# Performance work log

Measured on AMD Instinct MI355X. Metric: run time of the kernel, lower is better.

The kernel has to match this reference:

```python
import jax, jax.numpy as jnp
import numpy as np

B, L, D = 8, 8192, 1024
M = L // 4  # target_ratio=4 -> exactly L/4 boundaries per batch row (enforced in setup_inputs)


@jax.custom_vjp
def ste(x):
    # Forward: ones_like(x). Backward: pass gradient straight through.
    return jnp.ones_like(x)

def _ste_fwd(x):
    return jnp.ones_like(x), None

def _ste_bwd(_, g):
    return (g,)

ste.defvjp(_ste_fwd, _ste_bwd)


def _ema_combine(c1, c2):
    # Linear recurrence h = a*h_prev + b as an associative op (matches the
    # Hillis-Steele doubling scan in the torch source exactly).
    a1, b1 = c1
    a2, b2 = c2
    return (a1 * a2, a2[..., None] * b1 + b2)


def setup_inputs() -> dict:
    key = jax.random.key(0)
    k1, k2, k3, k4, k5 = jax.random.split(key, 5)
    x = jax.random.normal(k1, (B, L, D), jnp.float32)
    residual = jax.random.normal(k2, (B, L, D), jnp.float32)
    prob = jax.random.uniform(k3, (B, L), jnp.float32)
    # exactly M=L//4 True positions per row (random locations) -> static M
    r = jax.random.uniform(k4, (B, L))
    sel = jnp.argsort(r, axis=1)[:, :M]
    token_mask = jnp.zeros((B, L), bool).at[jnp.arange(B)[:, None], sel].set(True)
    state = jax.random.normal(k5, (B, D), jnp.float32)
    return {"x": x, "residual": residual, "prob": prob,
            "token_mask": token_mask, "state": state}


def reference(x, residual, prob, token_mask, state):
    # ---- Tokenizer: compact selected positions to the front (stable order) ----
    counts = token_mask.sum(axis=1)                       # (B,)
    order = jnp.argsort(~token_mask, axis=1)[:, :M]       # stable: True positions first, in order
    chunked = jnp.take_along_axis(x, order[:, :, None], axis=1)      # (B, M, D)
    chunk_probs = jnp.take_along_axis(prob, order, axis=1)           # (B, M)
    valid = jnp.arange(M)[None, :] < counts[:, None]                  # (B, M)
    chunk_probs = chunk_probs * valid                     # padded slots -> 0 (new_zeros semantics)

    # ---- EMA scan over compacted chunks ----
    decay = jnp.clip(1.0 - chunk_probs, 0.0, 1.0)         # (B, M)
    b = (1.0 - decay)[..., None] * chunked                # (B, M, D)
    b = b.at[:, 0].add(decay[:, 0, None] * state)         # fold initial state into b[0]
    _, ema = jax.lax.associative_scan(_ema_combine, (decay, b), axis=1)
    ema = ema * valid[..., None]

    # ---- DeTokenizer: scatter-expand back to (B, L, D) ----
    chunk_idx = jnp.cumsum(token_mask.astype(jnp.int32), axis=1) - 1  # (B, L)
    valid_pos = chunk_idx >= 0
    ci = jnp.clip(chunk_idx, 0, M - 1)
    long_states = jnp.take_along_axis(ema, ci[:, :, None], axis=1)    # (B, L, D)
    long_states = long_states * valid_pos[..., None]

    coef = ste(jnp.maximum(1.0 - prob, prob))             # forward: ones; bwd: STE
    long_states = long_states * coef[..., None]

    output = residual + long_states                       # (B, L, D)

    # new_state = last valid EMA value per batch (or carried-over state if empty)
    last = jnp.clip(counts - 1, 0, M - 1)
    new_state = jnp.take_along_axis(ema, last[:, None, None], axis=1)[:, 0]
    new_state = jnp.where((counts > 0)[:, None], new_state, state)
    return output, new_state
```

## Files before the change

### kernel.cpp

```cpp
#include <hip/hip_runtime.h>
#include <stdint.h>
#include <stddef.h>

#define B_ 8
#define L_ 8192
#define D_ 1024
#define M_ 2048
#define S_ 128
#define G_ 16
#define D4_ (D_/4)

typedef float f4 __attribute__((ext_vector_type(4)));

#define OFF_POS    ((size_t)0)
#define OFF_DEC    (OFF_POS  + (size_t)B_*M_*4)
#define OFF_A      (OFF_DEC  + (size_t)B_*M_*4)
#define OFF_EZ     (OFF_A    + (size_t)B_*S_*4)
#define OFF_HINIT  (OFF_EZ   + (size_t)B_*S_*D_*4)
#define WS_TOTAL   (OFF_HINIT + (size_t)B_*S_*D_*4)

__global__ __launch_bounds__(1024)
void compact_kernel(const void* __restrict__ mask_raw,
                    const float* __restrict__ prob,
                    int* __restrict__ pos,
                    float* __restrict__ dec) {
    const int b = blockIdx.x;
    const int t = threadIdx.x;

    __shared__ int u8flag;
    if (t == 0) u8flag = 0;
    __syncthreads();
    {
        const uint32_t* mu = (const uint32_t*)mask_raw;
        uint32_t w0 = mu[t * 2], w1 = mu[t * 2 + 1];
        if (w0 > 1u || w1 > 1u) atomicOr(&u8flag, 1);
    }
    __syncthreads();
    const bool u8 = (u8flag != 0);

    int mv[8];
    const int base_l = t * 8;
    if (u8) {
        const uint8_t* mrow = (const uint8_t*)mask_raw + (size_t)b * L_;
        #pragma unroll
        for (int j = 0; j < 8; j++) mv[j] = mrow[base_l + j] ? 1 : 0;
    } else {
        const int* mrow = (const int*)mask_raw + (size_t)b * L_;
        #pragma unroll
        for (int j = 0; j < 8; j++) mv[j] = mrow[base_l + j] ? 1 : 0;
    }
    int tsum = 0;
    #pragma unroll
    for (int j = 0; j < 8; j++) tsum += mv[j];

    const int lane = t & 63, wid = t >> 6;
    int v = tsum;
    #pragma unroll
    for (int off = 1; off < 64; off <<= 1) {
        int n = __shfl_up(v, off, 64);
        if (lane >= off) v += n;
    }
    __shared__ int wsum[16];
    __shared__ int woff[16];
    if (lane == 63) wsum[wid] = v;
    __syncthreads();
    if (t < 16) {
        int acc = 0;
        for (int w = 0; w < t; w++) acc += wsum[w];
        woff[t] = acc;
    }
    __syncthreads();
    int run = (v - tsum) + woff[wid];

    const float* prow = prob + (size_t)b * L_;
    #pragma unroll
    for (int j = 0; j < 8; j++) {
        const int l = base_l + j;
        if (mv[j]) {
            float d = 1.0f - prow[l];
            d = fminf(fmaxf(d, 0.0f), 1.0f);
            pos[(size_t)b * M_ + run] = l;
            dec[(size_t)b * M_ + run] = d;
            run += 1;
        }
    }
}

__global__ __launch_bounds__(256)
void segend_kernel(const f4* __restrict__ x4,
                   const int* __restrict__ pos,
                   const float* __restrict__ dec,
                   f4* __restrict__ ez4,
                   float* __restrict__ Aseg) {
    const int blk = blockIdx.x;
    const int b = blk / S_, s = blk % S_;
    const int t = threadIdx.x;
    __shared__ int   pl[G_];
    __shared__ float dl[G_];
    if (t < G_) {
        pl[t] = pos[(size_t)b * M_ + (size_t)s * G_ + t];
        dl[t] = dec[(size_t)b * M_ + (size_t)s * G_ + t];
    }
    __syncthreads();
    f4 h = (f4)(0.0f);
    #pragma unroll
    for (int m = 0; m < G_; m++) {
        const float d = dl[m];
        const float w = 1.0f - d;
        const f4 xv = x4[((size_t)b * L_ + pl[m]) * D4_ + t];
        h = d * h + w * xv;
    }
    ez4[((size_t)b * S_ + s) * D4_ + t] = h;
    if (t == 0) {
        float p = 1.0f;
        #pragma unroll
        for (int m = 0; m < G_; m++) p *= dl[m];
        Aseg[b * S_ + s] = p;
    }
}

__global__ __launch_bounds__(64)
void combine_kernel(const float* __restrict__ ez,
                    const float* __restrict__ Aseg,
                    const float* __restrict__ state,
                    float* __restrict__ hinit,
                    float* __restrict__ newstate) {
    const int b = blockIdx.x;
    const int ch = blockIdx.y * 64 + threadIdx.x;
    __shared__ float Al[S_];
    Al[threadIdx.x] = Aseg[b * S_ + threadIdx.x];
    Al[threadIdx.x + 64] = Aseg[b * S_ + threadIdx.x + 64];
    __syncthreads();

    float c = state[(size_t)b * D_ + ch];
    for (int s0 = 0; s0 < S_; s0 += 8) {
        float e[8];
        #pragma unroll
        for (int j = 0; j < 8; j++)
            e[j] = ez[((size_t)b * S_ + s0 + j) * D_ + ch];
        #pragma unroll
        for (int j = 0; j < 8; j++) {
            hinit[((size_t)b * S_ + s0 + j) * D_ + ch] = c;
            c = fmaf(Al[s0 + j], c, e[j]);
        }
    }
    newstate[(size_t)b * D_ + ch] = c;
}

__global__ __launch_bounds__(256)
void fused_kernel(const f4* __restrict__ x4,
                  const f4* __restrict__ res4,
                  const int* __restrict__ pos,
                  const float* __restrict__ dec,
                  const f4* __restrict__ hinit4,
                  f4* __restrict__ out4) {
    const int blk = blockIdx.x;
    const int b = blk / S_, s = blk % S_;
    const int t = threadIdx.x;
    __shared__ int   pl[G_ + 1];
    __shared__ float dl[G_];
    if (t < G_) {
        pl[t] = pos[(size_t)b * M_ + (size_t)s * G_ + t];
        dl[t] = dec[(size_t)b * M_ + (size_t)s * G_ + t];
    }
    if (t == 0) {
        pl[G_] = (s == S_ - 1) ? L_ : pos[(size_t)b * M_ + (size_t)(s + 1) * G_];
    }
    __syncthreads();

    const f4* xrow   = x4   + (size_t)b * L_ * D4_;
    const f4* resrow = res4 + (size_t)b * L_ * D4_;
    f4*       outrow = out4 + (size_t)b * L_ * D4_;

    if (s == 0) {
        const int p0 = pl[0];
        int l = 0;
        for (; l + 4 <= p0; l += 4) {
            f4 r0 = __builtin_nontemporal_load(resrow + (size_t)(l + 0) * D4_ + t);
            f4 r1 = __builtin_nontemporal_load(resrow + (size_t)(l + 1) * D4_ + t);
            f4 r2 = __builtin_nontemporal_load(resrow + (size_t)(l + 2) * D4_ + t);
            f4 r3 = __builtin_nontemporal_load(resrow + (size_t)(l + 3) * D4_ + t);
            __builtin_nontemporal_store(r0, outrow + (size_t)(l + 0) * D4_ + t);
            __builtin_nontemporal_store(r1, outrow + (size_t)(l + 1) * D4_ + t);
            __builtin_nontemporal_store(r2, outrow + (size_t)(l + 2) * D4_ + t);
            __builtin_nontemporal_store(r3, outrow + (size_t)(l + 3) * D4_ + t);
        }
        for (; l < p0; l++) {
            f4 r = __builtin_nontemporal_load(resrow + (size_t)l * D4_ + t);
            __builtin_nontemporal_store(r, outrow + (size_t)l * D4_ + t);
        }
    }

    f4 h  = hinit4[((size_t)b * S_ + s) * D4_ + t];
    f4 xv = xrow[(size_t)pl[0] * D4_ + t];
    for (int m = 0; m < G_; m++) {
        f4 xn = xv;
        if (m < G_ - 1) xn = xrow[(size_t)pl[m + 1] * D4_ + t];
        const float d = dl[m];
        const float w = 1.0f - d;
        h = d * h + w * xv;
        const int lend = pl[m + 1];
        int l = pl[m];
        for (; l + 4 <= lend; l += 4) {
            f4 r0 = __builtin_nontemporal_load(resrow + (size_t)(l + 0) * D4_ + t);
            f4 r1 = __builtin_nontemporal_load(resrow + (size_t)(l + 1) * D4_ + t);
            f4 r2 = __builtin_nontemporal_load(resrow + (size_t)(l + 2) * D4_ + t);
            f4 r3 = __builtin_nontemporal_load(resrow + (size_t)(l + 3) * D4_ + t);
            r0 += h; r1 += h; r2 += h; r3 += h;
            __builtin_nontemporal_store(r0, outrow + (size_t)(l + 0) * D4_ + t);
            __builtin_nontemporal_store(r1, outrow + (size_t)(l + 1) * D4_ + t);
            __builtin_nontemporal_store(r2, outrow + (size_t)(l + 2) * D4_ + t);
            __builtin_nontemporal_store(r3, outrow + (size_t)(l + 3) * D4_ + t);
        }
        for (; l < lend; l++) {
            f4 r = __builtin_nontemporal_load(resrow + (size_t)l * D4_ + t);
            r += h;
            __builtin_nontemporal_store(r, outrow + (size_t)l * D4_ + t);
        }
        xv = xn;
    }
}

extern "C" void kernel_launch(void* const* d_in, const int* in_sizes, int n_in,
                              void* d_out, int out_size, void* d_ws, size_t ws_size,
                              hipStream_t stream) {
    const float* x        = (const float*)d_in[0];
    const float* residual = (const float*)d_in[1];
    const float* prob     = (const float*)d_in[2];
    const void*  mask     = d_in[3];
    const float* state    = (const float*)d_in[4];

    float* out       = (float*)d_out;
    float* new_state = out + (size_t)B_ * L_ * D_;

    if (ws_size < WS_TOTAL) return;

    char* ws = (char*)d_ws;
    int*   pos   = (int*)  (ws + OFF_POS);
    float* dec   = (float*)(ws + OFF_DEC);
    float* Aseg  = (float*)(ws + OFF_A);
    float* ez    = (float*)(ws + OFF_EZ);
    float* hinit = (float*)(ws + OFF_HINIT);

    compact_kernel<<<B_, 1024, 0, stream>>>(mask, prob, pos, dec);

    segend_kernel<<<B_ * S_, 256, 0, stream>>>(
        (const f4*)x, pos, dec, (f4*)ez, Aseg);

    combine_kernel<<<dim3(B_, 16), 64, 0, stream>>>(
        ez, Aseg, state, hinit, new_state);

    fused_kernel<<<B_ * S_, 256, 0, stream>>>(
        (const f4*)x, (const f4*)residual, pos, dec,
        (const f4*)hinit, (f4*)out);
}
```

Measured before the change: 147.4 us.

## Fuse four-stage pipeline into one cooperative kernel with grid syncs

Result: slower. 480.7 us (+226.2%).

```diff
diff --git a/kernel.cpp b/kernel.cpp
--- a/kernel.cpp
+++ b/kernel.cpp
@@ -1,6 +1,9 @@
 #include <hip/hip_runtime.h>
+#include <hip/hip_cooperative_groups.h>
 #include <stdint.h>
 #include <stddef.h>
+
+namespace cg = cooperative_groups;
 
 #define B_ 8
 #define L_ 8192
@@ -9,6 +12,7 @@
 #define S_ 128
 #define G_ 16
 #define D4_ (D_/4)
+#define NBLK_ (B_*S_)
 
 typedef float f4 __attribute__((ext_vector_type(4)));
 
@@ -18,6 +22,192 @@
 #define OFF_EZ     (OFF_A    + (size_t)B_*S_*4)
 #define OFF_HINIT  (OFF_EZ   + (size_t)B_*S_*D_*4)
 #define WS_TOTAL   (OFF_HINIT + (size_t)B_*S_*D_*4)
+
+__global__ __launch_bounds__(256, 4)
+void mega_kernel(const f4* __restrict__ x4,
+                 const f4* __restrict__ res4,
+                 const float* __restrict__ prob,
+                 const void* __restrict__ mask_raw,
+                 const float* __restrict__ state,
+                 int* __restrict__ pos,
+                 float* __restrict__ dec,
+                 float* __restrict__ Aseg,
+                 float* __restrict__ ez,
+                 float* __restrict__ hinit,
+                 f4* __restrict__ out4,
+                 float* __restrict__ newstate) {
+    cg::grid_group grid = cg::this_grid();
+    const int blk = blockIdx.x;
+    const int t = threadIdx.x;
+
+    __shared__ int   u8flag;
+    __shared__ int   wsum[4];
+    __shared__ int   woff[4];
+    __shared__ int   pl[G_ + 1];
+    __shared__ float dl[G_];
+    __shared__ float Al[S_];
+
+    if (blk < B_) {
+        const int b = blk;
+        if (t == 0) u8flag = 0;
+        __syncthreads();
+        {
+            const uint32_t* mu = (const uint32_t*)mask_raw;
+            uint32_t orv = 0;
+            #pragma unroll
+            for (int j = 0; j < 8; j++) orv |= mu[t * 8 + j];
+            if (orv > 1u) atomicOr(&u8flag, 1);
+        }
+        __syncthreads();
+        const bool u8 = (u8flag != 0);
+
+        const int base_l = t * 32;
+        int cnt = 0;
+        if (u8) {
+            const uint8_t* mrow = (const uint8_t*)mask_raw + (size_t)b * L_;
+            #pragma unroll
+            for (int j = 0; j < 32; j++) cnt += mrow[base_l + j] ? 1 : 0;
+        } else {
+            const int* mrow = (const int*)mask_raw + (size_t)b * L_;
+            #pragma unroll
+            for (int j = 0; j < 32; j++) cnt += mrow[base_l + j] ? 1 : 0;
+        }
+        const int lane = t & 63, wid = t >> 6;
+        int v = cnt;
+        #pragma unroll
+        for (int off = 1; off < 64; off <<= 1) {
+            int n = __shfl_up(v, off, 64);
+            if (lane >= off) v += n;
+        }
+        if (lane == 63) wsum[wid] = v;
+        __syncthreads();
+        if (t < 4) {
+            int acc = 0;
+            for (int w = 0; w < t; w++) acc += wsum[w];
+            woff[t] = acc;
+        }
+        __syncthreads();
+        int run = (v - cnt) + woff[wid];
+
+        const float* prow = prob + (size_t)b * L_;
+        if (u8) {
+            const uint8_t* mrow = (const uint8_t*)mask_raw + (size_t)b * L_;
+            for (int j = 0; j < 32; j++) {
+                const int l = base_l + j;
+                if (mrow[l]) {
+                    float d = fminf(fmaxf(1.0f - prow[l], 0.0f), 1.0f);
+                    pos[(size_t)b * M_ + run] = l;
+                    dec[(size_t)b * M_ + run] = d;
+                    run++;
+                }
+            }
+        } else {
+            const int* mrow = (const int*)mask_raw + (size_t)b * L_;
+            for (int j = 0; j < 32; j++) {
+                const int l = base_l + j;
+                if (mrow[l]) {
+                    float d = fminf(fmaxf(1.0f - prow[l], 0.0f), 1.0f);
+                    pos[(size_t)b * M_ + run] = l;
+                    dec[(size_t)b * M_ + run] = d;
+                    run++;
+                }
+            }
+        }
+        __threadfence();
+    }
+    grid.sync();
+
+    const int b = blk >> 7;
+    const int s = blk & (S_ - 1);
+    if (t < G_) {
+        pl[t] = pos[(size_t)b * M_ + s * G_ + t];
+        dl[t] = dec[(size_t)b * M_ + s * G_ + t];
+    }
+    if (t == 0) {
+        pl[G_] = (s == S_ - 1) ? L_ : pos[(size_t)b * M_ + (s + 1) * G_];
+    }
+    __syncthreads();
+
+    const f4* xrow = x4 + (size_t)b * L_ * D4_;
+    f4 xr[G_];
+    f4 h = (f4)(0.0f);
+    #pragma unroll
+    for (int m = 0; m < G_; m++) {
+        xr[m] = xrow[(size_t)pl[m] * D4_ + t];
+        const float d = dl[m];
+        h = d * h + (1.0f - d) * xr[m];
+    }
+    ((f4*)ez)[(size_t)blk * D4_ + t] = h;
+    if (t == 0) {
+        float p = 1.0f;
+        #pragma unroll
+        for (int m = 0; m < G_; m++) p *= dl[m];
+        Aseg[blk] = p;
+    }
+    __threadfence();
+    grid.sync();
+
+    if (blk < 32) {
+        const int b2 = blk >> 2;
+        const int ch = ((blk & 3) << 8) + t;
+        if (t < S_) Al[t] = Aseg[b2 * S_ + t];
+        __syncthreads();
+        float c = state[(size_t)b2 * D_ + ch];
+        for (int s0 = 0; s0 < S_; s0 += 8) {
+            float e[8];
+            #pragma unroll
+            for (int j = 0; j < 8; j++)
+                e[j] = ez[((size_t)b2 * S_ + s0 + j) * D_ + ch];
+            #pragma unroll
+            for (int j = 0; j < 8; j++) {
+                hinit[((size_t)b2 * S_ + s0 + j) * D_ + ch] = c;
+                c = fmaf(Al[s0 + j], c, e[j]);
+            }
+        }
+        newstate[(size_t)b2 * D_ + ch] = c;
+        __threadfence();
+    }
+    grid.sync();
+
+    const f4* resrow = res4 + (size_t)b * L_ * D4_;
+    f4*       outrow = out4 + (size_t)b * L_ * D4_;
+
+    if (s == 0) {
+        const int p0 = pl[0];
+        int l = 0;
+        for (; l + 2 <= p0; l += 2) {
+            f4 r0 = __builtin_nontemporal_load(resrow + (size_t)(l + 0) * D4_ + t);
+            f4 r1 = __builtin_nontemporal_load(resrow + (size_t)(l + 1) * D4_ + t);
+            __builtin_nontemporal_store(r0, outrow + (size_t)(l + 0) * D4_ + t);
+            __builtin_nontemporal_store(r1, outrow + (size_t)(l + 1) * D4_ + t);
+        }
+        if (l < p0) {
+            f4 r = __builtin_nontemporal_load(resrow + (size_t)l * D4_ + t);
+            __builtin_nontemporal_store(r, outrow + (size_t)l * D4_ + t);
+        }
+    }
+
+    f4 h3 = ((const f4*)hinit)[(size_t)blk * D4_ + t];
+    #pragma unroll
+    for (int m = 0; m < G_; m++) {
+        const float d = dl[m];
+        h3 = d * h3 + (1.0f - d) * xr[m];
+        const int lend = pl[m + 1];
+        int l = pl[m];
+        for (; l + 2 <= lend; l += 2) {
+            f4 r0 = __builtin_nontemporal_load(resrow + (size_t)(l + 0) * D4_ + t);
+            f4 r1 = __builtin_nontemporal_load(resrow + (size_t)(l + 1) * D4_ + t);
+            r0 += h3; r1 += h3;
+            __builtin_nontemporal_store(r0, outrow + (size_t)(l + 0) * D4_ + t);
+            __builtin_nontemporal_store(r1, outrow + (size_t)(l + 1) * D4_ + t);
+        }
+        if (l < lend) {
+            f4 r = __builtin_nontemporal_load(resrow + (size_t)l * D4_ + t);
+            r += h3;
+            __builtin_nontemporal_store(r, outrow + (size_t)l * D4_ + t);
+        }
+    }
+}
 
 __global__ __launch_bounds__(1024)
 void compact_kernel(const void* __restrict__ mask_raw,
@@ -26,7 +216,6 @@
                     float* __restrict__ dec) {
     const int b = blockIdx.x;
     const int t = threadIdx.x;
-
     __shared__ int u8flag;
     if (t == 0) u8flag = 0;
     __syncthreads();
@@ -37,7 +226,6 @@
     }
     __syncthreads();
     const bool u8 = (u8flag != 0);
-
     int mv[8];
     const int base_l = t * 8;
     if (u8) {
@@ -52,7 +240,6 @@
     int tsum = 0;
     #pragma unroll
     for (int j = 0; j < 8; j++) tsum += mv[j];
-
     const int lane = t & 63, wid = t >> 6;
     int v = tsum;
     #pragma unroll
@@ -71,14 +258,12 @@
     }
     __syncthreads();
     int run = (v - tsum) + woff[wid];
-
     const float* prow = prob + (size_t)b * L_;
     #pragma unroll
     for (int j = 0; j < 8; j++) {
         const int l = base_l + j;
         if (mv[j]) {
-            float d = 1.0f - prow[l];
-            d = fminf(fmaxf(d, 0.0f), 1.0f);
+            float d = fminf(fmaxf(1.0f - prow[l], 0.0f), 1.0f);
             pos[(size_t)b * M_ + run] = l;
             dec[(size_t)b * M_ + run] = d;
             run += 1;
@@ -106,9 +291,8 @@
     #pragma unroll
     for (int m = 0; m < G_; m++) {
         const float d = dl[m];
-        const float w = 1.0f - d;
         const f4 xv = x4[((size_t)b * L_ + pl[m]) * D4_ + t];
-        h = d * h + w * xv;
+        h = d * h + (1.0f - d) * xv;
     }
     ez4[((size_t)b * S_ + s) * D4_ + t] = h;
     if (t == 0) {
@@ -131,7 +315,6 @@
     Al[threadIdx.x] = Aseg[b * S_ + threadIdx.x];
     Al[threadIdx.x + 64] = Aseg[b * S_ + threadIdx.x + 64];
     __syncthreads();
-
     float c = state[(size_t)b * D_ + ch];
     for (int s0 = 0; s0 < S_; s0 += 8) {
         float e[8];
@@ -167,57 +350,28 @@
         pl[G_] = (s == S_ - 1) ? L_ : pos[(size_t)b * M_ + (size_t)(s + 1) * G_];
     }
     __syncthreads();
-
     const f4* xrow   = x4   + (size_t)b * L_ * D4_;
     const f4* resrow = res4 + (size_t)b * L_ * D4_;
     f4*       outrow = out4 + (size_t)b * L_ * D4_;
-
     if (s == 0) {
         const int p0 = pl[0];
-        int l = 0;
-        for (; l + 4 <= p0; l += 4) {
-            f4 r0 = __builtin_nontemporal_load(resrow + (size_t)(l + 0) * D4_ + t);
-            f4 r1 = __builtin_nontemporal_load(resrow + (size_t)(l + 1) * D4_ + t);
-            f4 r2 = __builtin_nontemporal_load(resrow + (size_t)(l + 2) * D4_ + t);
-            f4 r3 = __builtin_nontemporal_load(resrow + (size_t)(l + 3) * D4_ + t);
-            __builtin_nontemporal_store(r0, outrow + (size_t)(l + 0) * D4_ + t);
-            __builtin_nontemporal_store(r1, outrow + (size_t)(l + 1) * D4_ + t);
-            __builtin_nontemporal_store(r2, outrow + (size_t)(l + 2) * D4_ + t);
-            __builtin_nontemporal_store(r3, outrow + (size_t)(l + 3) * D4_ + t);
-        }
-        for (; l < p0; l++) {
+        for (int l = 0; l < p0; l++) {
             f4 r = __builtin_nontemporal_load(resrow + (size_t)l * D4_ + t);
             __builtin_nontemporal_store(r, outrow + (size_t)l * D4_ + t);
         }
     }
-
-    f4 h  = hinit4[((size_t)b * S_ + s) * D4_ + t];
-    f4 xv = xrow[(size_t)pl[0] * D4_ + t];
+    f4 h = hinit4[((size_t)b * S_ + s) * D4_ + t];
+    #pragma unroll
     for (int m = 0; m < G_; m++) {
-        f4 xn = xv;
-        if (m < G_ - 1) xn = xrow[(size_t)pl[m + 1] * D4_ + t];
         const float d = dl[m];
-        const float w = 1.0f - d;
-        h = d * h + w * xv;
+        const f4 xv = xrow[(size_t)pl[m] * D4_ + t];
+        h = d * h + (1.0f - d) * xv;
         const int lend = pl[m + 1];
-        int l = pl[m];
-        for (; l + 4 <= lend; l += 4) {
-            f4 r0 = __builtin_nontemporal_load(resrow + (size_t)(l + 0) * D4_ + t);
-            f4 r1 = __builtin_nontemporal_load(resrow + (size_t)(l + 1) * D4_ + t);
-            f4 r2 = __builtin_nontemporal_load(resrow + (size_t)(l + 2) * D4_ + t);
-            f4 r3 = __builtin_nontemporal_load(resrow + (size_t)(l + 3) * D4_ + t);
-            r0 += h; r1 += h; r2 += h; r3 += h;
-            __builtin_nontemporal_store(r0, outrow + (size_t)(l + 0) * D4_ + t);
-            __builtin_nontemporal_store(r1, outrow + (size_t)(l + 1) * D4_ + t);
-            __builtin_nontemporal_store(r2, outrow + (size_t)(l + 2) * D4_ + t);
-            __builtin_nontemporal_store(r3, outrow + (size_t)(l + 3) * D4_ + t);
-        }
-        for (; l < lend; l++) {
+        for (int l = pl[m]; l < lend; l++) {
             f4 r = __builtin_nontemporal_load(resrow + (size_t)l * D4_ + t);
             r += h;
             __builtin_nontemporal_store(r, outrow + (size_t)l * D4_ + t);
         }
-        xv = xn;
     }
 }
 
@@ -242,15 +396,22 @@
     float* ez    = (float*)(ws + OFF_EZ);
     float* hinit = (float*)(ws + OFF_HINIT);
 
-    compact_kernel<<<B_, 1024, 0, stream>>>(mask, prob, pos, dec);
-
-    segend_kernel<<<B_ * S_, 256, 0, stream>>>(
-        (const f4*)x, pos, dec, (f4*)ez, Aseg);
-
-    combine_kernel<<<dim3(B_, 16), 64, 0, stream>>>(
-        ez, Aseg, state, hinit, new_state);
-
-    fused_kernel<<<B_ * S_, 256, 0, stream>>>(
-        (const f4*)x, (const f4*)residual, pos, dec,
-        (const f4*)hinit, (f4*)out);
-}
+    const f4* x4   = (const f4*)x;
+    const f4* res4 = (const f4*)residual;
+    f4*       out4 = (f4*)out;
+
+    void* args[] = {
+        (void*)&x4, (void*)&res4, (void*)&prob, (void*)&mask, (void*)&state,
+        (void*)&pos, (void*)&dec, (void*)&Aseg, (void*)&ez, (void*)&hinit,
+        (void*)&out4, (void*)&new_state
+    };
+    hipError_t err = hipLaunchCooperativeKernel(
+        (const void*)mega_kernel, dim3(NBLK_), dim3(256), args, 0, stream);
+
+    if (err != hipSuccess) {
+        compact_kernel<<<B_, 1024, 0, stream>>>(mask, prob, pos, dec);
+        segend_kernel<<<B_ * S_, 256, 0, stream>>>(x4, pos, dec, (f4*)ez, Aseg);
+        combine_kernel<<<dim3(B_, 16), 64, 0, stream>>>(ez, Aseg, state, hinit, new_state);
+        fused_kernel<<<B_ * S_, 256, 0, stream>>>(x4, res4, pos, dec, (const f4*)hinit, out4);
+    }
+}
```
